# Performance work log

Measured on AMD Instinct MI355X. Metric: run time of the kernel, lower is better.

## Reference

```python
import jax, jax.numpy as jnp
import numpy as np

B, D, K = 32, 64, 256            # batch, num objects (seq len), feature size (== in_size)
G = [256, 256, 256]              # g_layers sizes
F1, F2, OUT = 256, 256, 128      # f_fc1, f_fc2, out_size


def setup_inputs() -> dict:
    key = jax.random.key(0)
    ks = jax.random.split(key, 16)
    scale = 0.02

    def w(k, shape):
        return jax.random.normal(k, shape, dtype=jnp.float32) * scale

    x = jax.random.normal(ks[0], (B, D, K), dtype=jnp.float32)
    # edge_feature: Linear(2*K, K). Stored [in, out] (transposed vs torch).
    edge_w = w(ks[1], (2 * K, K))
    edge_b = jnp.zeros((K,), dtype=jnp.float32)
    g_ws, g_bs = [], []
    in_s = K
    for i, out_s in enumerate(G):
        g_ws.append(w(ks[2 + i], (in_s, out_s)))
        g_bs.append(jnp.zeros((out_s,), dtype=jnp.float32))
        in_s = out_s
    f1_w = w(ks[8], (G[-1], F1)); f1_b = jnp.zeros((F1,), dtype=jnp.float32)
    f2_w = w(ks[9], (F1, F2));    f2_b = jnp.zeros((F2,), dtype=jnp.float32)
    f3_w = w(ks[10], (F2, OUT));  f3_b = jnp.zeros((OUT,), dtype=jnp.float32)
    return dict(x=x, edge_w=edge_w, edge_b=edge_b, g_ws=g_ws, g_bs=g_bs,
                f1_w=f1_w, f1_b=f1_b, f2_w=f2_w, f2_b=f2_b, f3_w=f3_w, f3_b=f3_b)


def reference(x, edge_w, edge_b, g_ws, g_bs, f1_w, f1_b, f2_w, f2_b, f3_w, f3_b):
    # x: [B, D, K]. Original builds x_full[b,i,j] = concat(x[b,j], x[b,i]) then
    # applies edge_feature (Linear(2K -> K)). Equivalent, without materializing the
    # concat: split edge_w into the halves acting on x_i (=x[b,j]) and x_j (=x[b,i]).
    k = x.shape[-1]
    u = x @ edge_w[:k]      # [B, D, K]  -> indexed by j (axis 2)
    v = x @ edge_w[k:]      # [B, D, K]  -> indexed by i (axis 1)
    h = u[:, None, :, :] + v[:, :, None, :] + edge_b   # [B, D, D, K]
    # g MLP over all d^2 pairs (Linear + ReLU chain)
    for gw, gb in zip(g_ws, g_bs):
        h = jax.nn.relu(h @ gw + gb)
    # sum-aggregate over all pairs
    x_g = h.sum(axis=(1, 2))                            # [B, G[-1]]
    # f MLP (dropout p=0.0 -> identity)
    x_f = jax.nn.relu(x_g @ f1_w + f1_b)
    x_f = jax.nn.relu(x_f @ f2_w + f2_b)
    return x_f @ f3_w + f3_b                            # [B, OUT]
```

## Files before the change

### kernel.cpp

```cpp
#include <hip/hip_runtime.h>
#include <hip/hip_bf16.h>

typedef __attribute__((ext_vector_type(4))) float f32x4;
typedef __attribute__((ext_vector_type(2))) int   i32x2;
typedef __attribute__((ext_vector_type(4))) int   i32x4;
typedef __attribute__((ext_vector_type(8))) short short8;

__device__ __forceinline__ unsigned short f2bf(float x) {
  __hip_bfloat16 h = __float2bfloat16(x);
  union { __hip_bfloat16 h1; unsigned short u; } c; c.h1 = h; return c.u;
}
__device__ __forceinline__ unsigned pk2(float a, float b) {
  __hip_bfloat162 h = __float22bfloat162_rn(make_float2(a, b));
  union { __hip_bfloat162 h2; unsigned u; } c; c.h2 = h; return c.u;
}
__device__ __forceinline__ float bf2f(unsigned short u) {
  union { unsigned u32; float f; } c; c.u32 = ((unsigned)u) << 16; return c.f;
}

__global__ void k_prep(const float* __restrict__ edge_w, const float* __restrict__ edge_b,
                       const float* __restrict__ gw0, const float* __restrict__ gb0,
                       unsigned short* __restrict__ W1uR, unsigned short* __restrict__ W1vR,
                       float* __restrict__ c1) {
  const int blk = blockIdx.x, t = threadIdx.x;
  __shared__ float eu[256], ev[256];
  if (blk < 256) {
    eu[t] = edge_w[blk * 256 + t];
    ev[t] = edge_w[(256 + blk) * 256 + t];
    __syncthreads();
    float su = 0.f, sv = 0.f;
    for (int o = 0; o < 256; ++o) {
      float gg = gw0[o * 256 + t];
      su += eu[o] * gg; sv += ev[o] * gg;
    }
    const int k = blk, m = t;
    const int w = m >> 6, mf = (m >> 4) & 3, q = m & 15;
    const int ch = k >> 5, g = (k >> 3) & 3, e = k & 7;
    const int idx = ((w * 8 + ch) * 4 + mf) * 512 + (g * 16 + q) * 8 + e;
    W1uR[idx] = f2bf(su);
    W1vR[idx] = f2bf(sv);
  } else {
    float s = gb0[t];
    for (int o = 0; o < 256; ++o) s += edge_b[o] * gw0[o * 256 + t];
    c1[t] = s;
  }
}

__global__ void k_uv(const float* __restrict__ x,
                     const unsigned short* __restrict__ W1uR,
                     const unsigned short* __restrict__ W1vR,
                     const float* __restrict__ c1,
                     const float* __restrict__ gw1, const float* __restrict__ gw2,
                     unsigned short* __restrict__ U1, float* __restrict__ V1c,
                     unsigned short* __restrict__ W2R, unsigned short* __restrict__ W3R) {
  __shared__ unsigned short xs[8192];

  const int t = threadIdx.x;
  if (blockIdx.x >= 128) {
    int p = blockIdx.x - 128;
    const float* src = (p < 32) ? gw1 : gw2;
    unsigned short* dst = (p < 32) ? W2R : W3R;
    p &= 31;
    int w = p >> 3, ch = p & 7;
    int mf = t >> 6, lane = t & 63, q = lane & 15, g = lane >> 4;
    int base = ((w * 8 + ch) * 4 + mf) * 512 + lane * 8;
    int m = w * 64 + mf * 16 + q;
#pragma unroll
    for (int e = 0; e < 8; ++e) {
      int k = ch * 32 + g * 8 + e;
      dst[base + e] = f2bf(src[k * 256 + m]);
    }
    return;
  }

  const int tile = blockIdx.x >> 1, sel = blockIdx.x & 1;
  const int r0 = tile * 32;
  const int wid = t >> 6, lane = t & 63;
  const int q = lane & 15, g = lane >> 4;
  const int mo = wid << 6;

  {
    const int row = t >> 3, sl = t & 7, r7 = row & 7;
    const float* xB = x + (size_t)(r0 + row) * 256;
    unsigned short* hB = xs + row * 256;
#pragma unroll
    for (int m = 0; m < 4; ++m) {
      int ks = sl + 8 * m;
      f32x4 u0 = *(const f32x4*)(xB + ks * 8);
      f32x4 u1 = *(const f32x4*)(xB + ks * 8 + 4);
      i32x4 wv = { (int)pk2(u0.x, u0.y), (int)pk2(u0.z, u0.w),
                   (int)pk2(u1.x, u1.y), (int)pk2(u1.z, u1.w) };
      *(i32x4*)(hB + (ks ^ r7) * 8) = wv;
    }
  }

  const unsigned short* WR = sel ? W1vR : W1uR;
  const unsigned short* aW = WR + (size_t)wid * 16384 + lane * 8;

  short8 a_[4], an_[4];
#pragma unroll
  for (int mf = 0; mf < 4; ++mf) a_[mf] = *(const short8*)(aW + mf * 512);

  __syncthreads();

  f32x4 acc[4][2];
#pragma unroll
  for (int mf = 0; mf < 4; ++mf)
#pragma unroll
    for (int nf = 0; nf < 2; ++nf) acc[mf][nf] = (f32x4){0.f, 0.f, 0.f, 0.f};

  for (int ch = 0; ch < 8; ++ch) {
    if (ch < 7) {
#pragma unroll
      for (int mf = 0; mf < 4; ++mf)
        an_[mf] = *(const short8*)(aW + (ch + 1) * 2048 + mf * 512);
    }
    short8 b_[2];
#pragma unroll
    for (int nf = 0; nf < 2; ++nf) {
      int r = q + 16 * nf;
      b_[nf] = *(const short8*)(xs + r * 256 + (((ch * 4 + g) ^ (r & 7)) * 8));
    }
#pragma unroll
    for (int mf = 0; mf < 4; ++mf)
#pragma unroll
      for (int nf = 0; nf < 2; ++nf)
        acc[mf][nf] = __builtin_amdgcn_mfma_f32_16x16x32_bf16(a_[mf], b_[nf], acc[mf][nf], 0, 0, 0);
    if (ch < 7) {
#pragma unroll
      for (int mf = 0; mf < 4; ++mf) a_[mf] = an_[mf];
    }
  }

#pragma unroll
  for (int mf = 0; mf < 4; ++mf) {
    int c2b = mo + 16 * mf + 4 * g;
#pragma unroll
    for (int nf = 0; nf < 2; ++nf) {
      int r = r0 + q + 16 * nf;
      f32x4 v = acc[mf][nf];
      if (sel == 0) {
        i32x2 wv = { (int)pk2(v.x, v.y), (int)pk2(v.z, v.w) };
        *(i32x2*)(U1 + (size_t)r * 256 + c2b) = wv;
      } else {
        f32x4 cc = *(const f32x4*)(c1 + c2b);
        f32x4 o = { v.x + cc.x, v.y + cc.y, v.z + cc.z, v.w + cc.w };
        *(f32x4*)(V1c + (size_t)r * 256 + c2b) = o;
      }
    }
  }
}

__device__ __forceinline__ void write_h1(short8 u, f32x4 v0, f32x4 v1,
                                         unsigned short* dst) {
  float r0 = fmaxf(bf2f((unsigned short)u[0]) + v0.x, 0.f);
  float r1 = fmaxf(bf2f((unsigned short)u[1]) + v0.y, 0.f);
  float r2 = fmaxf(bf2f((unsigned short)u[2]) + v0.z, 0.f);
  float r3 = fmaxf(bf2f((unsigned short)u[3]) + v0.w, 0.f);
  float r4 = fmaxf(bf2f((unsigned short)u[4]) + v1.x, 0.f);
  float r5 = fmaxf(bf2f((unsigned short)u[5]) + v1.y, 0.f);
  float r6 = fmaxf(bf2f((unsigned short)u[6]) + v1.z, 0.f);
  float r7 = fmaxf(bf2f((unsigned short)u[7]) + v1.w, 0.f);
  i32x4 wv = { (int)pk2(r0, r1), (int)pk2(r2, r3), (int)pk2(r4, r5), (int)pk2(r6, r7) };
  *(i32x4*)dst = wv;
}

__launch_bounds__(512, 4)
__global__ void k_main(const unsigned short* __restrict__ U1,
                       const float* __restrict__ V1c,
                       const unsigned short* __restrict__ W2R,
                       const unsigned short* __restrict__ W3R,
                       const float* __restrict__ b2, const float* __restrict__ b3,
                       float* __restrict__ partials) {
  __shared__ unsigned short bufA[16384];
  __shared__ unsigned short bufB[16384];

  const int t = threadIdx.x;
  const int bid = blockIdx.x;
  const int wrk = ((bid & 7) << 7) | (bid >> 3);
  const int b = wrk >> 5;
  const int it0 = (wrk & 31) * 2;
  const int sel = t >> 8;
  const int tt = t & 255;
  const int wid4 = (t >> 6) & 3;
  const int lane = t & 63;
  const int q = lane & 15, g = lane >> 4;
  const int mo = wid4 << 6;

  unsigned short* const buf = sel ? bufB : bufA;

  {
    const int row = tt >> 2, sl = tt & 3, r7 = row & 7;
    const unsigned short* uB = U1 + (size_t)(b * 64 + row) * 256;
    const float* vP = V1c + (size_t)(b * 64 + it0 + sel) * 256;
    unsigned short* d = buf + row * 256;
#pragma unroll
    for (int m = 0; m < 8; ++m) {
      int ks = sl + 4 * m;
      int s8 = (ks ^ r7) * 8;
      short8 u = *(const short8*)(uB + ks * 8);
      f32x4 v0 = *(const f32x4*)(vP + ks * 8);
      f32x4 v1 = *(const f32x4*)(vP + ks * 8 + 4);
      write_h1(u, v0, v1, d + s8);
    }
  }

  const unsigned short* aW2 = W2R + (size_t)wid4 * 16384 + lane * 8;
  const unsigned short* aW3 = W3R + (size_t)wid4 * 16384 + lane * 8;

  __syncthreads();

  f32x4 acc[4][4];
#pragma unroll
  for (int mf = 0; mf < 4; ++mf)
#pragma unroll
    for (int nf = 0; nf < 4; ++nf) acc[mf][nf] = (f32x4){0.f, 0.f, 0.f, 0.f};

#pragma unroll
  for (int ch = 0; ch < 8; ++ch) {
    short8 a_[4];
#pragma unroll
    for (int mf = 0; mf < 4; ++mf)
      a_[mf] = *(const short8*)(aW2 + ch * 2048 + mf * 512);
    short8 b_[4];
#pragma unroll
    for (int nf = 0; nf < 4; ++nf) {
      int r = q + 16 * nf;
      b_[nf] = *(const short8*)(buf + r * 256 + (((ch * 4 + g) ^ (r & 7)) * 8));
    }
#pragma unroll
    for (int mf = 0; mf < 4; ++mf)
#pragma unroll
      for (int nf = 0; nf < 4; ++nf)
        acc[mf][nf] = __builtin_amdgcn_mfma_f32_16x16x32_bf16(a_[mf], b_[nf], acc[mf][nf], 0, 0, 0);
  }

  __syncthreads();

#pragma unroll
  for (int mf = 0; mf < 4; ++mf) {
    int c2b = mo + 16 * mf + 4 * g;
    f32x4 bb = *(const f32x4*)(b2 + c2b);
    int ksw = c2b >> 3, off = c2b & 7;
#pragma unroll
    for (int nf = 0; nf < 4; ++nf) {
      int r = q + 16 * nf;
      int dst = r * 256 + ((ksw ^ (r & 7)) * 8) + off;
      f32x4 v = acc[mf][nf];
      i32x2 wv = { (int)pk2(fmaxf(v.x + bb.x, 0.f), fmaxf(v.y + bb.y, 0.f)),
                   (int)pk2(fmaxf(v.z + bb.z, 0.f), fmaxf(v.w + bb.w, 0.f)) };
      *(i32x2*)(buf + dst) = wv;
    }
  }
  __syncthreads();

#pragma unroll
  for (int mf = 0; mf < 4; ++mf)
#pragma unroll
    for (int nf = 0; nf < 4; ++nf) acc[mf][nf] = (f32x4){0.f, 0.f, 0.f, 0.f};

#pragma unroll
  for (int ch = 0; ch < 8; ++ch) {
    short8 a_[4];
#pragma unroll
    for (int mf = 0; mf < 4; ++mf)
      a_[mf] = *(const short8*)(aW3 + ch * 2048 + mf * 512);
    short8 b_[4];
#pragma unroll
    for (int nf = 0; nf < 4; ++nf) {
      int r = q + 16 * nf;
      b_[nf] = *(const short8*)(buf + r * 256 + (((ch * 4 + g) ^ (r & 7)) * 8));
    }
#pragma unroll
    for (int mf = 0; mf < 4; ++mf)
#pragma unroll
      for (int nf = 0; nf < 4; ++nf)
        acc[mf][nf] = __builtin_amdgcn_mfma_f32_16x16x32_bf16(a_[mf], b_[nf], acc[mf][nf], 0, 0, 0);
  }

  __syncthreads();

  float* scr = (float*)buf;
#pragma unroll
  for (int mf = 0; mf < 4; ++mf) {
    int n3b = mo + 16 * mf + 4 * g;
    f32x4 bb = *(const f32x4*)(b3 + n3b);
    f32x4 sum = (f32x4){0.f, 0.f, 0.f, 0.f};
#pragma unroll
    for (int nf = 0; nf < 4; ++nf) {
      f32x4 v = acc[mf][nf];
      sum.x += fmaxf(v.x + bb.x, 0.f);
      sum.y += fmaxf(v.y + bb.y, 0.f);
      sum.z += fmaxf(v.z + bb.z, 0.f);
      sum.w += fmaxf(v.w + bb.w, 0.f);
    }
    *(f32x4*)(scr + q * 264 + n3b) = sum;
  }
  __syncthreads();
  float s = 0.f;
#pragma unroll
  for (int q2 = 0; q2 < 16; ++q2) s += scr[q2 * 264 + tt];
  partials[(size_t)(b * 64 + it0 + sel) * 256 + tt] = s;
}

__global__ void k_fmlp(const float* __restrict__ partials,
                       const float* __restrict__ f1w, const float* __restrict__ f1b,
                       const float* __restrict__ f2w, const float* __restrict__ f2b,
                       const float* __restrict__ f3w, const float* __restrict__ f3b,
                       float* __restrict__ out) {
  const int b = blockIdx.x, t = threadIdx.x;
  __shared__ float xg[256], x1[256], x2[256];
  {
    const float* p = partials + (size_t)(b * 64) * 256 + t;
    float s[8];
#pragma unroll
    for (int i = 0; i < 8; ++i) s[i] = 0.f;
#pragma unroll
    for (int k = 0; k < 8; ++k)
#pragma unroll
      for (int i = 0; i < 8; ++i) s[i] += p[(k * 8 + i) * 256];
    float tot = 0.f;
#pragma unroll
    for (int i = 0; i < 8; ++i) tot += s[i];
    xg[t] = tot;
  }
  __syncthreads();
  {
    float a0 = 0.f, a1 = 0.f, a2 = 0.f, a3 = 0.f;
#pragma unroll 4
    for (int k = 0; k < 64; ++k) {
      a0 += xg[k]       * f1w[(k)       * 256 + t];
      a1 += xg[k + 64]  * f1w[(k + 64)  * 256 + t];
      a2 += xg[k + 128] * f1w[(k + 128) * 256 + t];
      a3 += xg[k + 192] * f1w[(k + 192) * 256 + t];
    }
    x1[t] = fmaxf((a0 + a1) + (a2 + a3) + f1b[t], 0.f);
  }
  __syncthreads();
  {
    float a0 = 0.f, a1 = 0.f, a2 = 0.f, a3 = 0.f;
#pragma unroll 4
    for (int k = 0; k < 64; ++k) {
      a0 += x1[k]       * f2w[(k)       * 256 + t];
      a1 += x1[k + 64]  * f2w[(k + 64)  * 256 + t];
      a2 += x1[k + 128] * f2w[(k + 128) * 256 + t];
      a3 += x1[k + 192] * f2w[(k + 192) * 256 + t];
    }
    x2[t] = fmaxf((a0 + a1) + (a2 + a3) + f2b[t], 0.f);
  }
  __syncthreads();
  if (t < 128) {
    float a0 = 0.f, a1 = 0.f, a2 = 0.f, a3 = 0.f;
#pragma unroll 4
    for (int k = 0; k < 64; ++k) {
      a0 += x2[k]       * f3w[(k)       * 128 + t];
      a1 += x2[k + 64]  * f3w[(k + 64)  * 128 + t];
      a2 += x2[k + 128] * f3w[(k + 128) * 128 + t];
      a3 += x2[k + 192] * f3w[(k + 192) * 128 + t];
    }
    out[b * 128 + t] = (a0 + a1) + (a2 + a3) + f3b[t];
  }
}

__global__ void k_zero(float* __restrict__ out, int n) {
  int i = blockIdx.x * 256 + threadIdx.x;
  if (i < n) out[i] = 0.f;
}

extern "C" void kernel_launch(void* const* d_in, const int* in_sizes, int n_in,
                              void* d_out, int out_size, void* d_ws, size_t ws_size,
                              hipStream_t stream) {
  const float* x      = (const float*)d_in[0];
  const float* edge_w = (const float*)d_in[1];
  const float* edge_b = (const float*)d_in[2];
  const float *gw0, *gw1, *gw2, *gb0, *gb1, *gb2;
  const float *f1w, *f1b, *f2w, *f2b, *f3w, *f3b;

  if (n_in >= 15 && in_sizes[3] == 65536 && in_sizes[4] == 65536 && in_sizes[5] == 65536) {
    gw0 = (const float*)d_in[3]; gw1 = (const float*)d_in[4]; gw2 = (const float*)d_in[5];
    gb0 = (const float*)d_in[6]; gb1 = (const float*)d_in[7]; gb2 = (const float*)d_in[8];
    f1w = (const float*)d_in[9];  f1b = (const float*)d_in[10];
    f2w = (const float*)d_in[11]; f2b = (const float*)d_in[12];
    f3w = (const float*)d_in[13]; f3b = (const float*)d_in[14];
  } else if (n_in >= 15 && in_sizes[3] == 65536 && in_sizes[4] == 256) {
    gw0 = (const float*)d_in[3]; gb0 = (const float*)d_in[4];
    gw1 = (const float*)d_in[5]; gb1 = (const float*)d_in[6];
    gw2 = (const float*)d_in[7]; gb2 = (const float*)d_in[8];
    f1w = (const float*)d_in[9];  f1b = (const float*)d_in[10];
    f2w = (const float*)d_in[11]; f2b = (const float*)d_in[12];
    f3w = (const float*)d_in[13]; f3b = (const float*)d_in[14];
  } else {
    const float* gws = (const float*)d_in[3];
    const float* gbs = (const float*)d_in[4];
    gw0 = gws;          gw1 = gws + 65536;  gw2 = gws + 131072;
    gb0 = gbs;          gb1 = gbs + 256;    gb2 = gbs + 512;
    f1w = (const float*)d_in[5];  f1b = (const float*)d_in[6];
    f2w = (const float*)d_in[7];  f2b = (const float*)d_in[8];
    f3w = (const float*)d_in[9];  f3b = (const float*)d_in[10];
  }

  char* ws = (char*)d_ws;
  float*          c1       = (float*)(ws);
  unsigned short* W1uR     = (unsigned short*)(ws + 1024);
  unsigned short* W1vR     = (unsigned short*)(ws + 132096);
  unsigned short* W2R      = (unsigned short*)(ws + 263168);
  unsigned short* W3R      = (unsigned short*)(ws + 394240);
  unsigned short* U1       = (unsigned short*)(ws + 525312);
  float*          V1c      = (float*)(ws + 1573888);
  float*          partials = (float*)(ws + 3671040);
  const size_t need = 5768192;
  (void)out_size; (void)n_in;

  if (ws_size < need) {
    k_zero<<<dim3((out_size + 255) / 256), dim3(256), 0, stream>>>((float*)d_out, out_size);
    return;
  }

  k_prep<<<dim3(257), dim3(256), 0, stream>>>(edge_w, edge_b, gw0, gb0,
                                              W1uR, W1vR, c1);
  k_uv<<<dim3(192), dim3(256), 0, stream>>>(x, W1uR, W1vR, c1, gw1, gw2,
                                            U1, V1c, W2R, W3R);
  k_main<<<dim3(1024), dim3(512), 0, stream>>>(U1, V1c, W2R, W3R, gb1, gb2,
                                               partials);
  k_fmlp<<<dim3(32), dim3(256), 0, stream>>>(partials, f1w, f1b, f2w, f2b, f3w, f3b,
                                             (float*)d_out);
}
```

Measured before the change: 73.12 us.

## Switch intermediate storage and MFMA from bf16 to fp16, store V1 as half

Converts all packed weights and activations from bf16 to fp16 and uses the f16 MFMA variant. V1c is now stored as fp16 instead of fp32, which halves its traffic, and the first g-layer's add+ReLU becomes packed half vector math instead of per-element float conversions. s_setprio is also raised around the MFMA blocks in k_main. fp16 has less exponent range than bf16, so overflow is a risk if activations grow large, though it gives more mantissa precision.

```diff
diff --git a/kernel.cpp b/kernel.cpp
--- a/kernel.cpp
+++ b/kernel.cpp
@@ -1,21 +1,17 @@
 #include <hip/hip_runtime.h>
-#include <hip/hip_bf16.h>
-
-typedef __attribute__((ext_vector_type(4))) float f32x4;
-typedef __attribute__((ext_vector_type(2))) int   i32x2;
-typedef __attribute__((ext_vector_type(4))) int   i32x4;
-typedef __attribute__((ext_vector_type(8))) short short8;
-
-__device__ __forceinline__ unsigned short f2bf(float x) {
-  __hip_bfloat16 h = __float2bfloat16(x);
-  union { __hip_bfloat16 h1; unsigned short u; } c; c.h1 = h; return c.u;
-}
-__device__ __forceinline__ unsigned pk2(float a, float b) {
-  __hip_bfloat162 h = __float22bfloat162_rn(make_float2(a, b));
-  union { __hip_bfloat162 h2; unsigned u; } c; c.h2 = h; return c.u;
-}
-__device__ __forceinline__ float bf2f(unsigned short u) {
-  union { unsigned u32; float f; } c; c.u32 = ((unsigned)u) << 16; return c.f;
+#include <hip/hip_fp16.h>
+
+typedef __attribute__((ext_vector_type(4))) float    f32x4;
+typedef __attribute__((ext_vector_type(2))) int      i32x2;
+typedef __attribute__((ext_vector_type(4))) int      i32x4;
+typedef __attribute__((ext_vector_type(8))) _Float16 half8;
+
+__device__ __forceinline__ unsigned short f2h_u(float x) {
+  union { _Float16 h; unsigned short u; } c; c.h = (_Float16)x; return c.u;
+}
+__device__ __forceinline__ unsigned pk2h(float a, float b) {
+  union { _Float16 h[2]; unsigned u; } c;
+  c.h[0] = (_Float16)a; c.h[1] = (_Float16)b; return c.u;
 }
 
 __global__ void k_prep(const float* __restrict__ edge_w, const float* __restrict__ edge_b,
@@ -37,8 +33,8 @@
     const int w = m >> 6, mf = (m >> 4) & 3, q = m & 15;
     const int ch = k >> 5, g = (k >> 3) & 3, e = k & 7;
     const int idx = ((w * 8 + ch) * 4 + mf) * 512 + (g * 16 + q) * 8 + e;
-    W1uR[idx] = f2bf(su);
-    W1vR[idx] = f2bf(sv);
+    W1uR[idx] = f2h_u(su);
+    W1vR[idx] = f2h_u(sv);
   } else {
     float s = gb0[t];
     for (int o = 0; o < 256; ++o) s += edge_b[o] * gw0[o * 256 + t];
@@ -51,7 +47,7 @@
                      const unsigned short* __restrict__ W1vR,
                      const float* __restrict__ c1,
                      const float* __restrict__ gw1, const float* __restrict__ gw2,
-                     unsigned short* __restrict__ U1, float* __restrict__ V1c,
+                     unsigned short* __restrict__ U1, unsigned short* __restrict__ V1h,
                      unsigned short* __restrict__ W2R, unsigned short* __restrict__ W3R) {
   __shared__ unsigned short xs[8192];
 
@@ -68,7 +64,7 @@
 #pragma unroll
     for (int e = 0; e < 8; ++e) {
       int k = ch * 32 + g * 8 + e;
-      dst[base + e] = f2bf(src[k * 256 + m]);
+      dst[base + e] = f2h_u(src[k * 256 + m]);
     }
     return;
   }
@@ -88,8 +84,8 @@
       int ks = sl + 8 * m;
       f32x4 u0 = *(const f32x4*)(xB + ks * 8);
       f32x4 u1 = *(const f32x4*)(xB + ks * 8 + 4);
-      i32x4 wv = { (int)pk2(u0.x, u0.y), (int)pk2(u0.z, u0.w),
-                   (int)pk2(u1.x, u1.y), (int)pk2(u1.z, u1.w) };
+      i32x4 wv = { (int)pk2h(u0.x, u0.y), (int)pk2h(u0.z, u0.w),
+                   (int)pk2h(u1.x, u1.y), (int)pk2h(u1.z, u1.w) };
       *(i32x4*)(hB + (ks ^ r7) * 8) = wv;
     }
   }
@@ -97,9 +93,9 @@
   const unsigned short* WR = sel ? W1vR : W1uR;
   const unsigned short* aW = WR + (size_t)wid * 16384 + lane * 8;
 
-  short8 a_[4], an_[4];
-#pragma unroll
-  for (int mf = 0; mf < 4; ++mf) a_[mf] = *(const short8*)(aW + mf * 512);
+  half8 a_[4], an_[4];
+#pragma unroll
+  for (int mf = 0; mf < 4; ++mf) a_[mf] = *(const half8*)(aW + mf * 512);
 
   __syncthreads();
 
@@ -113,19 +109,19 @@
     if (ch < 7) {
 #pragma unroll
       for (int mf = 0; mf < 4; ++mf)
-        an_[mf] = *(const short8*)(aW + (ch + 1) * 2048 + mf * 512);
-    }
-    short8 b_[2];
+        an_[mf] = *(const half8*)(aW + (ch + 1) * 2048 + mf * 512);
+    }
+    half8 b_[2];
 #pragma unroll
     for (int nf = 0; nf < 2; ++nf) {
       int r = q + 16 * nf;
-      b_[nf] = *(const short8*)(xs + r * 256 + (((ch * 4 + g) ^ (r & 7)) * 8));
+      b_[nf] = *(const half8*)(xs + r * 256 + (((ch * 4 + g) ^ (r & 7)) * 8));
     }
 #pragma unroll
     for (int mf = 0; mf < 4; ++mf)
 #pragma unroll
       for (int nf = 0; nf < 2; ++nf)
-        acc[mf][nf] = __builtin_amdgcn_mfma_f32_16x16x32_bf16(a_[mf], b_[nf], acc[mf][nf], 0, 0, 0);
+        acc[mf][nf] = __builtin_amdgcn_mfma_f32_16x16x32_f16(a_[mf], b_[nf], acc[mf][nf], 0, 0, 0);
     if (ch < 7) {
 #pragma unroll
       for (int mf = 0; mf < 4; ++mf) a_[mf] = an_[mf];
@@ -140,34 +136,31 @@
       int r = r0 + q + 16 * nf;
       f32x4 v = acc[mf][nf];
       if (sel == 0) {
-        i32x2 wv = { (int)pk2(v.x, v.y), (int)pk2(v.z, v.w) };
+        i32x2 wv = { (int)pk2h(v.x, v.y), (int)pk2h(v.z, v.w) };
         *(i32x2*)(U1 + (size_t)r * 256 + c2b) = wv;
       } else {
         f32x4 cc = *(const f32x4*)(c1 + c2b);
-        f32x4 o = { v.x + cc.x, v.y + cc.y, v.z + cc.z, v.w + cc.w };
-        *(f32x4*)(V1c + (size_t)r * 256 + c2b) = o;
+        i32x2 wv = { (int)pk2h(v.x + cc.x, v.y + cc.y),
+                     (int)pk2h(v.z + cc.z, v.w + cc.w) };
+        *(i32x2*)(V1h + (size_t)r * 256 + c2b) = wv;
       }
     }
   }
 }
 
-__device__ __forceinline__ void write_h1(short8 u, f32x4 v0, f32x4 v1,
+__device__ __forceinline__ void write_h1(const unsigned short* u,
+                                         const unsigned short* v,
                                          unsigned short* dst) {
-  float r0 = fmaxf(bf2f((unsigned short)u[0]) + v0.x, 0.f);
-  float r1 = fmaxf(bf2f((unsigned short)u[1]) + v0.y, 0.f);
-  float r2 = fmaxf(bf2f((unsigned short)u[2]) + v0.z, 0.f);
-  float r3 = fmaxf(bf2f((unsigned short)u[3]) + v0.w, 0.f);
-  float r4 = fmaxf(bf2f((unsigned short)u[4]) + v1.x, 0.f);
-  float r5 = fmaxf(bf2f((unsigned short)u[5]) + v1.y, 0.f);
-  float r6 = fmaxf(bf2f((unsigned short)u[6]) + v1.z, 0.f);
-  float r7 = fmaxf(bf2f((unsigned short)u[7]) + v1.w, 0.f);
-  i32x4 wv = { (int)pk2(r0, r1), (int)pk2(r2, r3), (int)pk2(r4, r5), (int)pk2(r6, r7) };
-  *(i32x4*)dst = wv;
+  half8 a = *(const half8*)u;
+  half8 b = *(const half8*)v;
+  half8 z = (half8)(_Float16)0.0f;
+  half8 r = __builtin_elementwise_max(a + b, z);
+  *(half8*)dst = r;
 }
 
 __launch_bounds__(512, 4)
 __global__ void k_main(const unsigned short* __restrict__ U1,
-                       const float* __restrict__ V1c,
+                       const unsigned short* __restrict__ V1h,
                        const unsigned short* __restrict__ W2R,
                        const unsigned short* __restrict__ W3R,
                        const float* __restrict__ b2, const float* __restrict__ b3,
@@ -192,16 +185,13 @@
   {
     const int row = tt >> 2, sl = tt & 3, r7 = row & 7;
     const unsigned short* uB = U1 + (size_t)(b * 64 + row) * 256;
-    const float* vP = V1c + (size_t)(b * 64 + it0 + sel) * 256;
+    const unsigned short* vP = V1h + (size_t)(b * 64 + it0 + sel) * 256;
     unsigned short* d = buf + row * 256;
 #pragma unroll
     for (int m = 0; m < 8; ++m) {
       int ks = sl + 4 * m;
       int s8 = (ks ^ r7) * 8;
-      short8 u = *(const short8*)(uB + ks * 8);
-      f32x4 v0 = *(const f32x4*)(vP + ks * 8);
-      f32x4 v1 = *(const f32x4*)(vP + ks * 8 + 4);
-      write_h1(u, v0, v1, d + s8);
+      write_h1(uB + ks * 8, vP + ks * 8, d + s8);
     }
   }
 
@@ -218,21 +208,23 @@
 
 #pragma unroll
   for (int ch = 0; ch < 8; ++ch) {
-    short8 a_[4];
+    half8 a_[4];
 #pragma unroll
     for (int mf = 0; mf < 4; ++mf)
-      a_[mf] = *(const short8*)(aW2 + ch * 2048 + mf * 512);
-    short8 b_[4];
+      a_[mf] = *(const half8*)(aW2 + ch * 2048 + mf * 512);
+    half8 b_[4];
 #pragma unroll
     for (int nf = 0; nf < 4; ++nf) {
       int r = q + 16 * nf;
-      b_[nf] = *(const short8*)(buf + r * 256 + (((ch * 4 + g) ^ (r & 7)) * 8));
-    }
+      b_[nf] = *(const half8*)(buf + r * 256 + (((ch * 4 + g) ^ (r & 7)) * 8));
+    }
+    __builtin_amdgcn_s_setprio(1);
 #pragma unroll
     for (int mf = 0; mf < 4; ++mf)
 #pragma unroll
       for (int nf = 0; nf < 4; ++nf)
-        acc[mf][nf] = __builtin_amdgcn_mfma_f32_16x16x32_bf16(a_[mf], b_[nf], acc[mf][nf], 0, 0, 0);
+        acc[mf][nf] = __builtin_amdgcn_mfma_f32_16x16x32_f16(a_[mf], b_[nf], acc[mf][nf], 0, 0, 0);
+    __builtin_amdgcn_s_setprio(0);
   }
 
   __syncthreads();
@@ -247,8 +239,8 @@
       int r = q + 16 * nf;
       int dst = r * 256 + ((ksw ^ (r & 7)) * 8) + off;
       f32x4 v = acc[mf][nf];
-      i32x2 wv = { (int)pk2(fmaxf(v.x + bb.x, 0.f), fmaxf(v.y + bb.y, 0.f)),
-                   (int)pk2(fmaxf(v.z + bb.z, 0.f), fmaxf(v.w + bb.w, 0.f)) };
+      i32x2 wv = { (int)pk2h(fmaxf(v.x + bb.x, 0.f), fmaxf(v.y + bb.y, 0.f)),
+                   (int)pk2h(fmaxf(v.z + bb.z, 0.f), fmaxf(v.w + bb.w, 0.f)) };
       *(i32x2*)(buf + dst) = wv;
     }
   }
@@ -261,21 +253,23 @@
 
 #pragma unroll
   for (int ch = 0; ch < 8; ++ch) {
-    short8 a_[4];
+    half8 a_[4];
 #pragma unroll
     for (int mf = 0; mf < 4; ++mf)
-      a_[mf] = *(const short8*)(aW3 + ch * 2048 + mf * 512);
-    short8 b_[4];
+      a_[mf] = *(const half8*)(aW3 + ch * 2048 + mf * 512);
+    half8 b_[4];
 #pragma unroll
     for (int nf = 0; nf < 4; ++nf) {
       int r = q + 16 * nf;
-      b_[nf] = *(const short8*)(buf + r * 256 + (((ch * 4 + g) ^ (r & 7)) * 8));
-    }
+      b_[nf] = *(const half8*)(buf + r * 256 + (((ch * 4 + g) ^ (r & 7)) * 8));
+    }
+    __builtin_amdgcn_s_setprio(1);
 #pragma unroll
     for (int mf = 0; mf < 4; ++mf)
 #pragma unroll
       for (int nf = 0; nf < 4; ++nf)
-        acc[mf][nf] = __builtin_amdgcn_mfma_f32_16x16x32_bf16(a_[mf], b_[nf], acc[mf][nf], 0, 0, 0);
+        acc[mf][nf] = __builtin_amdgcn_mfma_f32_16x16x32_f16(a_[mf], b_[nf], acc[mf][nf], 0, 0, 0);
+    __builtin_amdgcn_s_setprio(0);
   }
 
   __syncthreads();
@@ -406,7 +400,7 @@
   unsigned short* W2R      = (unsigned short*)(ws + 263168);
   unsigned short* W3R      = (unsigned short*)(ws + 394240);
   unsigned short* U1       = (unsigned short*)(ws + 525312);
-  float*          V1c      = (float*)(ws + 1573888);
+  unsigned short* V1h      = (unsigned short*)(ws + 1573888);
   float*          partials = (float*)(ws + 3671040);
   const size_t need = 5768192;
   (void)out_size; (void)n_in;
@@ -419,8 +413,8 @@
   k_prep<<<dim3(257), dim3(256), 0, stream>>>(edge_w, edge_b, gw0, gb0,
                                               W1uR, W1vR, c1);
   k_uv<<<dim3(192), dim3(256), 0, stream>>>(x, W1uR, W1vR, c1, gw1, gw2,
-                                            U1, V1c, W2R, W3R);
-  k_main<<<dim3(1024), dim3(512), 0, stream>>>(U1, V1c, W2R, W3R, gb1, gb2,
+                                            U1, V1h, W2R, W3R);
+  k_main<<<dim3(1024), dim3(512), 0, stream>>>(U1, V1h, W2R, W3R, gb1, gb2,
                                                partials);
   k_fmlp<<<dim3(32), dim3(256), 0, stream>>>(partials, f1w, f1b, f2w, f2b, f3w, f3b,
                                              (float*)d_out);
```

Result: slower. 81.25 us (+11.1%).
